# Kernel optimization log

Hardware: AMD Instinct MI355X
Metric: run time of the kernel (lower is better)

The kernel has to match this reference:

```python
import jax, jax.numpy as jnp
import numpy as np

# config constants (from snn_toolbox config)
V_THRESH = 1.0      # cell.v_thresh
TAU_REFRAC = 0.1    # cell.tau_refrac (>0 -> refractory path active)
DT = 1.0            # simulation.dt
SHAPE = (32, 128, 64, 64)  # (batch, C, H, W) layer output shape


def setup_inputs() -> dict:
    key = jax.random.key(0)
    k1, k2, k3 = jax.random.split(key, 3)
    impulse = jax.random.normal(k1, SHAPE, dtype=jnp.float32)
    mem = 0.5 * jax.random.normal(k2, SHAPE, dtype=jnp.float32)
    # refractory-end times in [0, 2); with time=1.0 about half are refractory
    refrac_until = 2.0 * jax.random.uniform(k3, SHAPE, dtype=jnp.float32)
    payloads = jnp.zeros(SHAPE, jnp.float32)
    payloads_sum = jnp.zeros(SHAPE, jnp.float32)
    spikecounts = jnp.zeros(SHAPE, jnp.float32)
    time = jnp.ones((1,), jnp.float32)  # current simulation time
    return {"impulse": impulse, "mem": mem, "refrac_until": refrac_until,
            "payloads": payloads, "payloads_sum": payloads_sum,
            "spikecounts": spikecounts, "time": time}


def reference(impulse, mem, refrac_until, payloads, payloads_sum, spikecounts, time):
    """One timestep of SpikeLayer.update_neurons with linear_activation,
    'Reset by subtraction', payloads=True, online_normalization=True.
    Scatter ops (set_subtensor/inc_subtensor at spike indices) are the
    equivalent dense masked writes (jnp.where), same math."""
    t = time[0]
    dtype = mem.dtype
    # get_new_mem: zero input for neurons still refractory
    masked_impulse = jnp.where(refrac_until > t, jnp.zeros((), dtype), impulse)
    new_mem = mem + masked_impulse
    # linear activation: spike where membrane crosses threshold
    spiked = new_mem >= V_THRESH
    output_spikes = spiked.astype(dtype) * V_THRESH
    # set_reset_mem, 'Reset by subtraction' (pos and neg spikes)
    pos = output_spikes > 0
    neg = output_spikes < 0  # never true for linear activation, kept faithful
    mem_out = new_mem - V_THRESH * pos.astype(dtype) + V_THRESH * neg.astype(dtype)
    # payloads: residual of membrane after spike, at spike indices only
    residuals = new_mem - V_THRESH
    payloads_out = jnp.where(spiked, residuals - payloads_sum, payloads)
    payloads_sum_out = jnp.where(spiked, payloads_sum + payloads_out, payloads_sum)
    # refractory: spiking neurons become refractory until t + tau_refrac
    refrac_out = jnp.where(spiked, t + TAU_REFRAC, refrac_until)
    # online normalization bookkeeping
    spikecounts_out = spikecounts + spiked.astype(dtype)
    max_spikerate = jnp.max(spikecounts_out) * DT / t
    # spiketrain records spike time
    spiketrain = t * spiked.astype(dtype)
    return (output_spikes, mem_out, refrac_out, payloads_out,
            payloads_sum_out, spikecounts_out, spiketrain, max_spikerate)
```

## Files before the change

### kernel.cpp

```cpp
#include <hip/hip_runtime.h>

#define V_THRESH 1.0f
#define TAU_REFRAC 0.1f

__device__ __forceinline__ unsigned int map_f32(float f) {
    unsigned int u = __float_as_uint(f);
    return (u & 0x80000000u) ? ~u : (u | 0x80000000u);
}

__global__ void init_max_kernel(unsigned int* ws_max) {
    *ws_max = 0u;
}

__device__ __forceinline__ void neuron(float imp, float me, float rf,
                                       float pl, float ps, float sc,
                                       float t, float t_refrac_end,
                                       float& o_sp, float& o_mem, float& o_rf,
                                       float& o_pl, float& o_ps, float& o_sc,
                                       float& o_st, float& lmax) {
    float mi = (rf > t) ? 0.0f : imp;
    float nm = me + mi;
    bool spiked = (nm >= V_THRESH);
    float sp = spiked ? 1.0f : 0.0f;
    o_sp  = sp * V_THRESH;
    o_mem = nm - V_THRESH * sp;
    float resid = nm - V_THRESH;
    float new_pl = resid - ps;
    o_pl = spiked ? new_pl : pl;
    o_ps = spiked ? (ps + new_pl) : ps;
    o_rf = spiked ? t_refrac_end : rf;
    o_sc = sc + sp;
    o_st = t * sp;
    lmax = fmaxf(lmax, o_sc);
}

__global__ __launch_bounds__(256) void spike_kernel(
    const float4* __restrict__ impulse,
    const float4* __restrict__ mem,
    const float4* __restrict__ refrac,
    const float4* __restrict__ payloads,
    const float4* __restrict__ paysum,
    const float4* __restrict__ spikecounts,
    const float* __restrict__ time,
    float4* __restrict__ out,
    unsigned int* __restrict__ ws_max,
    int n4)
{
    const float t = time[0];
    const float t_end = t + TAU_REFRAC;

    float4* __restrict__ o_sp  = out;
    float4* __restrict__ o_mem = out + (size_t)n4;
    float4* __restrict__ o_rf  = out + 2 * (size_t)n4;
    float4* __restrict__ o_pl  = out + 3 * (size_t)n4;
    float4* __restrict__ o_ps  = out + 4 * (size_t)n4;
    float4* __restrict__ o_sc  = out + 5 * (size_t)n4;
    float4* __restrict__ o_st  = out + 6 * (size_t)n4;

    float lmax = -__builtin_inff();
    const size_t stride = (size_t)gridDim.x * blockDim.x;
    for (size_t i = (size_t)blockIdx.x * blockDim.x + threadIdx.x;
         i < (size_t)n4; i += stride) {
        float4 im = impulse[i];
        float4 me = mem[i];
        float4 rf = refrac[i];
        float4 pl = payloads[i];
        float4 ps = paysum[i];
        float4 sc = spikecounts[i];
        float4 vsp, vmem, vrf, vpl, vps, vsc, vst;

        neuron(im.x, me.x, rf.x, pl.x, ps.x, sc.x, t, t_end,
               vsp.x, vmem.x, vrf.x, vpl.x, vps.x, vsc.x, vst.x, lmax);
        neuron(im.y, me.y, rf.y, pl.y, ps.y, sc.y, t, t_end,
               vsp.y, vmem.y, vrf.y, vpl.y, vps.y, vsc.y, vst.y, lmax);
        neuron(im.z, me.z, rf.z, pl.z, ps.z, sc.z, t, t_end,
               vsp.z, vmem.z, vrf.z, vpl.z, vps.z, vsc.z, vst.z, lmax);
        neuron(im.w, me.w, rf.w, pl.w, ps.w, sc.w, t, t_end,
               vsp.w, vmem.w, vrf.w, vpl.w, vps.w, vsc.w, vst.w, lmax);

        o_sp[i]  = vsp;
        o_mem[i] = vmem;
        o_rf[i]  = vrf;
        o_pl[i]  = vpl;
        o_ps[i]  = vps;
        o_sc[i]  = vsc;
        o_st[i]  = vst;
    }

    #pragma unroll
    for (int off = 32; off > 0; off >>= 1)
        lmax = fmaxf(lmax, __shfl_xor(lmax, off));
    if ((threadIdx.x & 63) == 0)
        atomicMax(ws_max, map_f32(lmax));
}

__global__ void finalize_kernel(const unsigned int* __restrict__ ws_max,
                                const float* __restrict__ time,
                                float* __restrict__ out_scalar) {
    unsigned int m = *ws_max;
    unsigned int u = (m & 0x80000000u) ? (m & 0x7fffffffu) : ~m;
    float v = __uint_as_float(u);
    out_scalar[0] = v * (1.0f / time[0]);
}

extern "C" void kernel_launch(void* const* d_in, const int* in_sizes, int n_in,
                              void* d_out, int out_size, void* d_ws, size_t ws_size,
                              hipStream_t stream) {
    const float4* impulse     = (const float4*)d_in[0];
    const float4* mem         = (const float4*)d_in[1];
    const float4* refrac      = (const float4*)d_in[2];
    const float4* payloads    = (const float4*)d_in[3];
    const float4* paysum      = (const float4*)d_in[4];
    const float4* spikecounts = (const float4*)d_in[5];
    const float*  time        = (const float*)d_in[6];

    const int n  = in_sizes[0];
    const int n4 = n / 4;
    float* out = (float*)d_out;
    unsigned int* ws_max = (unsigned int*)d_ws;

    init_max_kernel<<<1, 1, 0, stream>>>(ws_max);
    spike_kernel<<<2048, 256, 0, stream>>>(impulse, mem, refrac, payloads,
                                           paysum, spikecounts, time,
                                           (float4*)out, ws_max, n4);
    finalize_kernel<<<1, 1, 0, stream>>>(ws_max, time, out + 7 * (size_t)n);
}
```

Measured before the change: 190.5 us.

## Use nontemporal vector loads/stores and fuse finalize into main kernel via last-block ticket

Main loads and stores now use nontemporal builtins on ext_vector float4 types. The grid-stride loop is restructured into a fixed iteration count followed by a tail, to keep the loop simple. The separate finalize kernel is removed: the last block to finish, found by an atomic ticket counter, computes the max spikerate scalar. This saves one kernel launch and aims to cut cache pollution on a purely streaming workload, at the cost of an extra atomic and fence per block.

```diff
diff --git a/kernel.cpp b/kernel.cpp
--- a/kernel.cpp
+++ b/kernel.cpp
@@ -1,4 +1,6 @@
 #include <hip/hip_runtime.h>
+
+typedef float f32x4 __attribute__((ext_vector_type(4)));
 
 #define V_THRESH 1.0f
 #define TAU_REFRAC 0.1f
@@ -7,121 +9,142 @@
     unsigned int u = __float_as_uint(f);
     return (u & 0x80000000u) ? ~u : (u | 0x80000000u);
 }
-
-__global__ void init_max_kernel(unsigned int* ws_max) {
-    *ws_max = 0u;
+__device__ __forceinline__ float unmap_f32(unsigned int m) {
+    unsigned int u = (m & 0x80000000u) ? (m & 0x7fffffffu) : ~m;
+    return __uint_as_float(u);
 }
 
-__device__ __forceinline__ void neuron(float imp, float me, float rf,
-                                       float pl, float ps, float sc,
-                                       float t, float t_refrac_end,
-                                       float& o_sp, float& o_mem, float& o_rf,
-                                       float& o_pl, float& o_ps, float& o_sc,
-                                       float& o_st, float& lmax) {
-    float mi = (rf > t) ? 0.0f : imp;
-    float nm = me + mi;
-    bool spiked = (nm >= V_THRESH);
-    float sp = spiked ? 1.0f : 0.0f;
-    o_sp  = sp * V_THRESH;
-    o_mem = nm - V_THRESH * sp;
-    float resid = nm - V_THRESH;
-    float new_pl = resid - ps;
-    o_pl = spiked ? new_pl : pl;
-    o_ps = spiked ? (ps + new_pl) : ps;
-    o_rf = spiked ? t_refrac_end : rf;
-    o_sc = sc + sp;
-    o_st = t * sp;
-    lmax = fmaxf(lmax, o_sc);
+__global__ void init_ws_kernel(unsigned int* ws) {
+    ws[0] = 0u;
+    ws[1] = 0u;
+}
+
+__device__ __forceinline__ void neuron4(const f32x4 im, const f32x4 me,
+                                        const f32x4 rf, const f32x4 pl,
+                                        const f32x4 ps, const f32x4 sc,
+                                        float t, float t_end,
+                                        f32x4& vsp, f32x4& vmem, f32x4& vrf,
+                                        f32x4& vpl, f32x4& vps, f32x4& vsc,
+                                        f32x4& vst, float& lmax) {
+    #pragma unroll
+    for (int j = 0; j < 4; ++j) {
+        float imp = im[j], m0 = me[j], r0 = rf[j];
+        float p0 = pl[j], s0 = ps[j], c0 = sc[j];
+        float mi = (r0 > t) ? 0.0f : imp;
+        float nm = m0 + mi;
+        bool spiked = (nm >= V_THRESH);
+        float sp = spiked ? 1.0f : 0.0f;
+        float resid = nm - V_THRESH;
+        float new_pl = resid - s0;
+        vsp[j]  = sp * V_THRESH;
+        vmem[j] = nm - V_THRESH * sp;
+        vpl[j]  = spiked ? new_pl : p0;
+        vps[j]  = spiked ? (s0 + new_pl) : s0;
+        vrf[j]  = spiked ? t_end : r0;
+        float c1 = c0 + sp;
+        vsc[j]  = c1;
+        vst[j]  = t * sp;
+        lmax = fmaxf(lmax, c1);
+    }
 }
 
 __global__ __launch_bounds__(256) void spike_kernel(
-    const float4* __restrict__ impulse,
-    const float4* __restrict__ mem,
-    const float4* __restrict__ refrac,
-    const float4* __restrict__ payloads,
-    const float4* __restrict__ paysum,
-    const float4* __restrict__ spikecounts,
+    const f32x4* __restrict__ impulse,
+    const f32x4* __restrict__ mem,
+    const f32x4* __restrict__ refrac,
+    const f32x4* __restrict__ payloads,
+    const f32x4* __restrict__ paysum,
+    const f32x4* __restrict__ spikecounts,
     const float* __restrict__ time,
-    float4* __restrict__ out,
-    unsigned int* __restrict__ ws_max,
+    f32x4* __restrict__ out,
+    float* __restrict__ out_scalar,
+    unsigned int* __restrict__ ws,
     int n4)
 {
     const float t = time[0];
     const float t_end = t + TAU_REFRAC;
 
-    float4* __restrict__ o_sp  = out;
-    float4* __restrict__ o_mem = out + (size_t)n4;
-    float4* __restrict__ o_rf  = out + 2 * (size_t)n4;
-    float4* __restrict__ o_pl  = out + 3 * (size_t)n4;
-    float4* __restrict__ o_ps  = out + 4 * (size_t)n4;
-    float4* __restrict__ o_sc  = out + 5 * (size_t)n4;
-    float4* __restrict__ o_st  = out + 6 * (size_t)n4;
+    f32x4* __restrict__ o_sp  = out;
+    f32x4* __restrict__ o_mem = out + (size_t)n4;
+    f32x4* __restrict__ o_rf  = out + 2 * (size_t)n4;
+    f32x4* __restrict__ o_pl  = out + 3 * (size_t)n4;
+    f32x4* __restrict__ o_ps  = out + 4 * (size_t)n4;
+    f32x4* __restrict__ o_sc  = out + 5 * (size_t)n4;
+    f32x4* __restrict__ o_st  = out + 6 * (size_t)n4;
 
     float lmax = -__builtin_inff();
-    const size_t stride = (size_t)gridDim.x * blockDim.x;
-    for (size_t i = (size_t)blockIdx.x * blockDim.x + threadIdx.x;
-         i < (size_t)n4; i += stride) {
-        float4 im = impulse[i];
-        float4 me = mem[i];
-        float4 rf = refrac[i];
-        float4 pl = payloads[i];
-        float4 ps = paysum[i];
-        float4 sc = spikecounts[i];
-        float4 vsp, vmem, vrf, vpl, vps, vsc, vst;
+    const long stride = (long)gridDim.x * blockDim.x;
+    long i = (long)blockIdx.x * blockDim.x + threadIdx.x;
+    const long niter = (long)n4 / stride;
 
-        neuron(im.x, me.x, rf.x, pl.x, ps.x, sc.x, t, t_end,
-               vsp.x, vmem.x, vrf.x, vpl.x, vps.x, vsc.x, vst.x, lmax);
-        neuron(im.y, me.y, rf.y, pl.y, ps.y, sc.y, t, t_end,
-               vsp.y, vmem.y, vrf.y, vpl.y, vps.y, vsc.y, vst.y, lmax);
-        neuron(im.z, me.z, rf.z, pl.z, ps.z, sc.z, t, t_end,
-               vsp.z, vmem.z, vrf.z, vpl.z, vps.z, vsc.z, vst.z, lmax);
-        neuron(im.w, me.w, rf.w, pl.w, ps.w, sc.w, t, t_end,
-               vsp.w, vmem.w, vrf.w, vpl.w, vps.w, vsc.w, vst.w, lmax);
+    #pragma unroll 1
+    for (long k = 0; k < niter; ++k, i += stride) {
+        f32x4 im = __builtin_nontemporal_load(&impulse[i]);
+        f32x4 me = __builtin_nontemporal_load(&mem[i]);
+        f32x4 rf = __builtin_nontemporal_load(&refrac[i]);
+        f32x4 pl = __builtin_nontemporal_load(&payloads[i]);
+        f32x4 ps = __builtin_nontemporal_load(&paysum[i]);
+        f32x4 sc = __builtin_nontemporal_load(&spikecounts[i]);
+        f32x4 vsp, vmem, vrf, vpl, vps, vsc, vst;
 
-        o_sp[i]  = vsp;
-        o_mem[i] = vmem;
-        o_rf[i]  = vrf;
-        o_pl[i]  = vpl;
-        o_ps[i]  = vps;
-        o_sc[i]  = vsc;
-        o_st[i]  = vst;
+        neuron4(im, me, rf, pl, ps, sc, t, t_end,
+                vsp, vmem, vrf, vpl, vps, vsc, vst, lmax);
+
+        __builtin_nontemporal_store(vsp,  &o_sp[i]);
+        __builtin_nontemporal_store(vmem, &o_mem[i]);
+        __builtin_nontemporal_store(vrf,  &o_rf[i]);
+        __builtin_nontemporal_store(vpl,  &o_pl[i]);
+        __builtin_nontemporal_store(vps,  &o_ps[i]);
+        __builtin_nontemporal_store(vsc,  &o_sc[i]);
+        __builtin_nontemporal_store(vst,  &o_st[i]);
+    }
+    if (i < (long)n4) {
+        f32x4 im = impulse[i], me = mem[i], rf = refrac[i];
+        f32x4 pl = payloads[i], ps = paysum[i], sc = spikecounts[i];
+        f32x4 vsp, vmem, vrf, vpl, vps, vsc, vst;
+        neuron4(im, me, rf, pl, ps, sc, t, t_end,
+                vsp, vmem, vrf, vpl, vps, vsc, vst, lmax);
+        o_sp[i] = vsp; o_mem[i] = vmem; o_rf[i] = vrf; o_pl[i] = vpl;
+        o_ps[i] = vps; o_sc[i] = vsc; o_st[i] = vst;
     }
 
     #pragma unroll
     for (int off = 32; off > 0; off >>= 1)
         lmax = fmaxf(lmax, __shfl_xor(lmax, off));
     if ((threadIdx.x & 63) == 0)
-        atomicMax(ws_max, map_f32(lmax));
-}
+        atomicMax(&ws[0], map_f32(lmax));
 
-__global__ void finalize_kernel(const unsigned int* __restrict__ ws_max,
-                                const float* __restrict__ time,
-                                float* __restrict__ out_scalar) {
-    unsigned int m = *ws_max;
-    unsigned int u = (m & 0x80000000u) ? (m & 0x7fffffffu) : ~m;
-    float v = __uint_as_float(u);
-    out_scalar[0] = v * (1.0f / time[0]);
+    __syncthreads();
+    if (threadIdx.x == 0) {
+        __threadfence();
+        unsigned int ticket = atomicAdd(&ws[1], 1u);
+        if (ticket == gridDim.x - 1) {
+            __threadfence();
+            unsigned int m = atomicMax(&ws[0], 0u);
+            out_scalar[0] = unmap_f32(m) * (1.0f / t);
+        }
+    }
 }
 
 extern "C" void kernel_launch(void* const* d_in, const int* in_sizes, int n_in,
                               void* d_out, int out_size, void* d_ws, size_t ws_size,
                               hipStream_t stream) {
-    const float4* impulse     = (const float4*)d_in[0];
-    const float4* mem         = (const float4*)d_in[1];
-    const float4* refrac      = (const float4*)d_in[2];
-    const float4* payloads    = (const float4*)d_in[3];
-    const float4* paysum      = (const float4*)d_in[4];
-    const float4* spikecounts = (const float4*)d_in[5];
-    const float*  time        = (const float*)d_in[6];
+    const f32x4* impulse     = (const f32x4*)d_in[0];
+    const f32x4* mem         = (const f32x4*)d_in[1];
+    const f32x4* refrac      = (const f32x4*)d_in[2];
+    const f32x4* payloads    = (const f32x4*)d_in[3];
+    const f32x4* paysum      = (const f32x4*)d_in[4];
+    const f32x4* spikecounts = (const f32x4*)d_in[5];
+    const float* time        = (const float*)d_in[6];
 
     const int n  = in_sizes[0];
     const int n4 = n / 4;
     float* out = (float*)d_out;
-    unsigned int* ws_max = (unsigned int*)d_ws;
+    unsigned int* ws = (unsigned int*)d_ws;
 
-    init_max_kernel<<<1, 1, 0, stream>>>(ws_max);
+    init_ws_kernel<<<1, 1, 0, stream>>>(ws);
     spike_kernel<<<2048, 256, 0, stream>>>(impulse, mem, refrac, payloads,
                                            paysum, spikecounts, time,
-                                           (float4*)out, ws_max, n4);
-    finalize_kernel<<<1, 1, 0, stream>>>(ws_max, time, out + 7 * (size_t)n);
+                                           (f32x4*)out, out + 7 * (size_t)n,
+                                           ws, n4);
 }
```

Measured after the change: 281.0 us. 1.48x slower.
